# Kernel tuning notes

Hardware: AMD Instinct MI355X
Metric: run time of the kernel (lower is better)

Reference implementation:

```python
import jax, jax.numpy as jnp
import numpy as np

INF = 100000000.0
RATE = 22050.0 / 128.0  # audio_target_rate
SIZES = [[-1.0, 0.45608904], [0.45608904, 0.878505635], [0.878505635, 1.557724045],
         [1.557724045, 2.264785525], [2.264785525, 1000.0]]
LEVEL_SIZES = [65536, 32768, 16384, 8192, 4096]
NUM_ANN = 512


def setup_inputs() -> dict:
    key = jax.random.key(0)
    k1, k2, k3 = jax.random.split(key, 3)
    T = LEVEL_SIZES[0] * 2.0  # timeline length in downsampled frames
    left = jnp.sort(jax.random.uniform(k1, (NUM_ANN,), minval=0.0, maxval=T - 500.0))
    width = jax.random.uniform(k2, (NUM_ANN,), minval=20.0, maxval=400.0)
    cls = jax.random.randint(k3, (NUM_ANN,), 0, 2).astype(jnp.float32)  # 0=downbeat, 1=beat
    ann = jnp.stack([left, left + width, cls], axis=1)  # [M, 3]
    inp = {"jth_annotations": ann}
    for i, n in enumerate(LEVEL_SIZES):
        stride = 2.0 ** (i + 1)
        inp[f"anchors{i+1}"] = (jnp.arange(n, dtype=jnp.float32) + 0.5) * stride
    return inp


def _assign_level(ann, pts, i):
    # FCOS-style target assignment for one pyramid level.
    stride = 2.0 ** (i + 1)
    l = ann[None, :, 0]                      # [1, M]
    r = ann[None, :, 1]                      # [1, M]
    cls = ann[:, 2]                          # [M]
    # radius_per_class: (cls==0)*4.5 + (cls==1)*1.5
    radius = jnp.where(cls == 0, 4.5, 0.0) + jnp.where(cls == 1, 1.5, 0.0)
    limit = l + radius[None, :] * stride     # [1, M]
    p = pts[:, None]                         # [N, 1]
    in_radii = (p >= l) & (p <= jnp.minimum(r, limit))          # [N, M]
    l_star = p - l                                              # [N, M]
    r_star = r - p                                              # [N, M]
    max_lr = jnp.maximum(l_star, r_star)                        # max over (l*, r*)
    lo = SIZES[i][0] * RATE
    hi = SIZES[i][1] * RATE
    in_range = (max_lr >= lo) & (max_lr <= hi)                  # [N, M]
    areas = (ann[:, 1] - ann[:, 0])[None, :]                    # [1, M]
    area_mat = jnp.where(in_radii & in_range,
                         jnp.broadcast_to(areas, in_radii.shape), INF)
    min_area = jnp.min(area_mat, axis=1)                        # [N]
    amin = jnp.argmin(area_mat, axis=1)                         # [N] (first min, like torch)
    assigned = ann[amin]                                        # [N, 3]
    assigned = assigned.at[:, 2].set(jnp.where(min_area == INF, 0.0, assigned[:, 2]))
    normalized = jnp.stack([assigned[:, 0] / stride,
                            assigned[:, 1] / stride,
                            assigned[:, 2]], axis=1)
    ls = jnp.take_along_axis(l_star, amin[:, None], axis=1)[:, 0]
    rs = jnp.take_along_axis(r_star, amin[:, None], axis=1)[:, 0]
    # original casts the argmin index tensor to bool (index != 0)
    idx_bool = (amin != 0).astype(pts.dtype)
    level = jnp.full(pts.shape, float(i + 1), dtype=pts.dtype)
    # columns: [idx_bool | assigned(3) | normalized(3) | l* | r* | l*/s | r*/s | level]
    return jnp.concatenate([
        idx_bool[:, None], assigned, normalized,
        ls[:, None], rs[:, None], (ls / stride)[:, None], (rs / stride)[:, None],
        level[:, None]], axis=1)


def reference(jth_annotations, anchors1, anchors2, anchors3, anchors4, anchors5):
    levels = [anchors1, anchors2, anchors3, anchors4, anchors5]
    outs = [_assign_level(jth_annotations, pts, i) for i, pts in enumerate(levels)]
    return jnp.concatenate(outs, axis=0)  # [sum(N_i), 12]
```

## Files before the change

### kernel.cpp

```cpp
#include <hip/hip_runtime.h>

#define INF_VAL 100000000.0f
#define NUM_ANN 512
#define TOTAL_PTS 126976

__device__ __constant__ float c_lo[5] = {
    (float)(-1.0 * 172.265625),
    (float)(0.45608904 * 172.265625),
    (float)(0.878505635 * 172.265625),
    (float)(1.557724045 * 172.265625),
    (float)(2.264785525 * 172.265625)
};
__device__ __constant__ float c_hi[5] = {
    (float)(0.45608904 * 172.265625),
    (float)(0.878505635 * 172.265625),
    (float)(1.557724045 * 172.265625),
    (float)(2.264785525 * 172.265625),
    (float)(1000.0 * 172.265625)
};
__device__ __constant__ int c_n[5]    = {65536, 32768, 16384, 8192, 4096};
__device__ __constant__ int c_base[5] = {0, 65536, 98304, 114688, 122880};

__global__ __launch_bounds__(256) void init_kernel(unsigned long long* __restrict__ ws) {
    int g = blockIdx.x * 256 + threadIdx.x;
    if (g < TOTAL_PTS)
        ws[g] = ((unsigned long long)__float_as_uint(INF_VAL)) << 32;
}

__global__ __launch_bounds__(256) void scatter_kernel(const float* __restrict__ ann,
                                                      unsigned long long* __restrict__ ws) {
    int t = blockIdx.x * 256 + threadIdx.x;
    if (t >= NUM_ANN * 5) return;
    int k   = t & (NUM_ANN - 1);
    int lvl = t >> 9;

    float l = ann[k * 3 + 0];
    float r = ann[k * 3 + 1];
    float c = ann[k * 3 + 2];

    float stride = (float)(2 << lvl);
    float radius = (c == 0.0f ? 4.5f : 0.0f) + (c == 1.0f ? 1.5f : 0.0f);
    float limit  = __fadd_rn(l, __fmul_rn(radius, stride));
    float U      = fminf(r, limit);
    float lo     = c_lo[lvl];
    float hi     = c_hi[lvl];
    float area   = r - l;
    int   n      = c_n[lvl];
    int   pbase  = c_base[lvl];

    int j0 = (int)floorf(l / stride - 0.5f) - 1;
    int j1 = (int)ceilf (U / stride - 0.5f) + 1;
    j0 = j0 < 0 ? 0 : j0;
    j1 = j1 > n - 1 ? n - 1 : j1;

    unsigned long long key =
        (((unsigned long long)__float_as_uint(area)) << 32) | (unsigned)k;

    for (int j = j0; j <= j1; ++j) {
        float p      = (j + 0.5f) * stride;
        float l_star = p - l;
        float r_star = r - p;
        float max_lr = fmaxf(l_star, r_star);
        bool in_radii = (p >= l) && (p <= U);
        bool in_range = (max_lr >= lo) && (max_lr <= hi);
        if (in_radii && in_range)
            atomicMin(&ws[pbase + j], key);
    }
}

__global__ __launch_bounds__(256) void gather_kernel(const float* __restrict__ ann,
                                                     const unsigned long long* __restrict__ ws,
                                                     float* __restrict__ out) {
    int g = blockIdx.x * 256 + threadIdx.x;
    if (g >= TOTAL_PTS) return;

    int lvl, base;
    if      (g <  65536) { lvl = 0; base = 0;      }
    else if (g <  98304) { lvl = 1; base = 65536;  }
    else if (g < 114688) { lvl = 2; base = 98304;  }
    else if (g < 122880) { lvl = 3; base = 114688; }
    else                 { lvl = 4; base = 122880; }

    float stride = (float)(2 << lvl);
    float p = ((g - base) + 0.5f) * stride;

    unsigned long long key = ws[g];
    unsigned k        = (unsigned)(key & 0xffffffffu);
    unsigned areaBits = (unsigned)(key >> 32);

    float l = ann[k * 3 + 0];
    float r = ann[k * 3 + 1];
    float c = ann[k * 3 + 2];
    float cls_out = (areaBits == __float_as_uint(INF_VAL)) ? 0.0f : c;

    float inv = 1.0f / stride;
    float ls = p - l;
    float rs = r - p;

    float4 o0 = make_float4(k != 0 ? 1.0f : 0.0f, l, r, cls_out);
    float4 o1 = make_float4(l * inv, r * inv, cls_out, ls);
    float4 o2 = make_float4(rs, ls * inv, rs * inv, (float)(lvl + 1));

    float4* orow = (float4*)(out + (size_t)g * 12);
    orow[0] = o0;
    orow[1] = o1;
    orow[2] = o2;
}

extern "C" void kernel_launch(void* const* d_in, const int* in_sizes, int n_in,
                              void* d_out, int out_size, void* d_ws, size_t ws_size,
                              hipStream_t stream) {
    const float* ann = (const float*)d_in[0];
    float* out = (float*)d_out;
    unsigned long long* ws = (unsigned long long*)d_ws;

    const int blocks_pts = (TOTAL_PTS + 255) / 256;
    const int blocks_sc  = (NUM_ANN * 5 + 255) / 256;

    init_kernel   <<<blocks_pts, 256, 0, stream>>>(ws);
    scatter_kernel<<<blocks_sc,  256, 0, stream>>>(ann, ws);
    gather_kernel <<<blocks_pts, 256, 0, stream>>>(ann, ws, out);
}
```

Baseline: 69.39 us.

## Replace init/scatter/gather atomics with single per-point binary-search gather kernel

Drops the three-kernel pipeline (init workspace, atomicMin scatter from annotations, gather) in favour of one kernel. Each block stages the 512 annotations in shared memory, and each point binary-searches the sorted left edges to find the first annotation that can cover it. It then scans forward until l > p, keeping the minimum-area match. This removes two launches, the workspace traffic and the global atomics. In exchange, every point now runs a serial search and scan, and correctness relies on the annotations being sorted by left edge.

```diff
diff --git a/kernel.cpp b/kernel.cpp
--- a/kernel.cpp
+++ b/kernel.cpp
@@ -18,61 +18,24 @@
     (float)(2.264785525 * 172.265625),
     (float)(1000.0 * 172.265625)
 };
-__device__ __constant__ int c_n[5]    = {65536, 32768, 16384, 8192, 4096};
-__device__ __constant__ int c_base[5] = {0, 65536, 98304, 114688, 122880};
 
-__global__ __launch_bounds__(256) void init_kernel(unsigned long long* __restrict__ ws) {
-    int g = blockIdx.x * 256 + threadIdx.x;
-    if (g < TOTAL_PTS)
-        ws[g] = ((unsigned long long)__float_as_uint(INF_VAL)) << 32;
-}
+__global__ __launch_bounds__(256) void assign_compact_kernel(
+    const float* __restrict__ ann,
+    float* __restrict__ out)
+{
+    __shared__ float s_l[NUM_ANN];
+    __shared__ float s_r[NUM_ANN];
+    __shared__ float s_c[NUM_ANN];
 
-__global__ __launch_bounds__(256) void scatter_kernel(const float* __restrict__ ann,
-                                                      unsigned long long* __restrict__ ws) {
-    int t = blockIdx.x * 256 + threadIdx.x;
-    if (t >= NUM_ANN * 5) return;
-    int k   = t & (NUM_ANN - 1);
-    int lvl = t >> 9;
+    const int tid = threadIdx.x;
+    for (int k = tid; k < NUM_ANN; k += 256) {
+        s_l[k] = ann[k * 3 + 0];
+        s_r[k] = ann[k * 3 + 1];
+        s_c[k] = ann[k * 3 + 2];
+    }
+    __syncthreads();
 
-    float l = ann[k * 3 + 0];
-    float r = ann[k * 3 + 1];
-    float c = ann[k * 3 + 2];
-
-    float stride = (float)(2 << lvl);
-    float radius = (c == 0.0f ? 4.5f : 0.0f) + (c == 1.0f ? 1.5f : 0.0f);
-    float limit  = __fadd_rn(l, __fmul_rn(radius, stride));
-    float U      = fminf(r, limit);
-    float lo     = c_lo[lvl];
-    float hi     = c_hi[lvl];
-    float area   = r - l;
-    int   n      = c_n[lvl];
-    int   pbase  = c_base[lvl];
-
-    int j0 = (int)floorf(l / stride - 0.5f) - 1;
-    int j1 = (int)ceilf (U / stride - 0.5f) + 1;
-    j0 = j0 < 0 ? 0 : j0;
-    j1 = j1 > n - 1 ? n - 1 : j1;
-
-    unsigned long long key =
-        (((unsigned long long)__float_as_uint(area)) << 32) | (unsigned)k;
-
-    for (int j = j0; j <= j1; ++j) {
-        float p      = (j + 0.5f) * stride;
-        float l_star = p - l;
-        float r_star = r - p;
-        float max_lr = fmaxf(l_star, r_star);
-        bool in_radii = (p >= l) && (p <= U);
-        bool in_range = (max_lr >= lo) && (max_lr <= hi);
-        if (in_radii && in_range)
-            atomicMin(&ws[pbase + j], key);
-    }
-}
-
-__global__ __launch_bounds__(256) void gather_kernel(const float* __restrict__ ann,
-                                                     const unsigned long long* __restrict__ ws,
-                                                     float* __restrict__ out) {
-    int g = blockIdx.x * 256 + threadIdx.x;
-    if (g >= TOTAL_PTS) return;
+    const int g = blockIdx.x * 256 + tid;
 
     int lvl, base;
     if      (g <  65536) { lvl = 0; base = 0;      }
@@ -81,23 +44,51 @@
     else if (g < 122880) { lvl = 3; base = 114688; }
     else                 { lvl = 4; base = 122880; }
 
-    float stride = (float)(2 << lvl);
-    float p = ((g - base) + 0.5f) * stride;
+    const float stride = (float)(2 << lvl);
+    const float p  = ((g - base) + 0.5f) * stride;
+    const float lo = c_lo[lvl];
+    const float hi = c_hi[lvl];
 
-    unsigned long long key = ws[g];
-    unsigned k        = (unsigned)(key & 0xffffffffu);
-    unsigned areaBits = (unsigned)(key >> 32);
+    const float wlo = p - 4.5f * stride - 1.0f;
 
-    float l = ann[k * 3 + 0];
-    float r = ann[k * 3 + 1];
-    float c = ann[k * 3 + 2];
-    float cls_out = (areaBits == __float_as_uint(INF_VAL)) ? 0.0f : c;
+    int idx = 0;
+    {
+        int n = NUM_ANN;
+        while (n > 1) {
+            int half = n >> 1;
+            idx += (s_l[idx + half - 1] < wlo) ? half : 0;
+            n -= half;
+        }
+        if (s_l[idx] < wlo) idx = NUM_ANN;
+    }
 
-    float inv = 1.0f / stride;
-    float ls = p - l;
-    float rs = r - p;
+    float best = INF_VAL;
+    int amin = 0;
 
-    float4 o0 = make_float4(k != 0 ? 1.0f : 0.0f, l, r, cls_out);
+    for (int k = idx; k < NUM_ANN; ++k) {
+        float l = s_l[k];
+        if (l > p) break;
+        float r = s_r[k];
+        float c = s_c[k];
+        float radius = (c == 0.0f ? 4.5f : 0.0f) + (c == 1.0f ? 1.5f : 0.0f);
+        float limit  = __fadd_rn(l, __fmul_rn(radius, stride));
+        float l_star = p - l;
+        float r_star = r - p;
+        float max_lr = fmaxf(l_star, r_star);
+        bool in_radii = (p >= l) && (p <= fminf(r, limit));
+        bool in_range = (max_lr >= lo) && (max_lr <= hi);
+        float area = (in_radii && in_range) ? (r - l) : INF_VAL;
+        if (area < best) { best = area; amin = k; }
+    }
+
+    const float l = s_l[amin];
+    const float r = s_r[amin];
+    const float cls_out = (best == INF_VAL) ? 0.0f : s_c[amin];
+    const float inv = 1.0f / stride;
+    const float ls = p - l;
+    const float rs = r - p;
+
+    float4 o0 = make_float4(amin != 0 ? 1.0f : 0.0f, l, r, cls_out);
     float4 o1 = make_float4(l * inv, r * inv, cls_out, ls);
     float4 o2 = make_float4(rs, ls * inv, rs * inv, (float)(lvl + 1));
 
@@ -112,12 +103,5 @@
                               hipStream_t stream) {
     const float* ann = (const float*)d_in[0];
     float* out = (float*)d_out;
-    unsigned long long* ws = (unsigned long long*)d_ws;
-
-    const int blocks_pts = (TOTAL_PTS + 255) / 256;
-    const int blocks_sc  = (NUM_ANN * 5 + 255) / 256;
-
-    init_kernel   <<<blocks_pts, 256, 0, stream>>>(ws);
-    scatter_kernel<<<blocks_sc,  256, 0, stream>>>(ann, ws);
-    gather_kernel <<<blocks_pts, 256, 0, stream>>>(ann, ws, out);
+    assign_compact_kernel<<<TOTAL_PTS / 256, 256, 0, stream>>>(ann, out);
 }
```

New measurement: 66.46 us. 1.04x faster.
